# Kernel optimization log

Measured on AMD Instinct MI355X. Metric: run time of the kernel, lower is better.

## Reference

```python
import jax, jax.numpy as jnp
import numpy as np
import math

B, T, D, N = 4, 2048, 1024, 16
HD = D // N
SCALE = math.sqrt(D)  # source scales by sqrt(d_key) = sqrt(full model dim)
BIG = 1e9

def setup_inputs() -> dict:
    key = jax.random.key(0)
    ks = jax.random.split(key, 11)
    s = 1.0 / math.sqrt(D)
    return {
        "query": jax.random.normal(ks[0], (B, T, D), jnp.float32),
        "key": jax.random.normal(ks[1], (B, T, D), jnp.float32),
        "value": jax.random.normal(ks[2], (B, T, D), jnp.float32),
        "wq_w": jax.random.normal(ks[3], (D, D), jnp.float32) * s,
        "wq_b": jnp.zeros((D,), jnp.float32),
        "wk_w": jax.random.normal(ks[4], (D, D), jnp.float32) * s,
        "wk_b": jnp.zeros((D,), jnp.float32),
        "wv_w": jax.random.normal(ks[5], (D, D), jnp.float32) * s,
        "wv_b": jnp.zeros((D,), jnp.float32),
        "wo_w": jax.random.normal(ks[6], (D, D), jnp.float32) * s,
        "wo_b": jnp.zeros((D,), jnp.float32),
    }

def reference(query, key, value, wq_w, wq_b, wk_w, wk_b, wv_w, wv_b, wo_w, wo_b):
    # projections (torch Linear equiv; weights stored as (in,out))
    q = query @ wq_w + wq_b
    k = key @ wk_w + wk_b
    v = value @ wv_w + wv_b
    # split heads: (B,T,D) -> (B,N,T,HD)
    def split(x):
        return x.reshape(B, T, N, HD).transpose(0, 2, 1, 3)
    q, k, v = split(q), split(k), split(v)
    # dot products (source does elementwise mul+sum == einsum)
    scores = jnp.einsum('bnqd,bnkd->bnqk', q, k)
    # only_attend_front: subtract 1e9 on strict upper triangle
    tri = jnp.triu(jnp.ones((T, T), scores.dtype), 1) * BIG
    scores = scores - tri
    logits = scores / SCALE
    probs = jax.nn.softmax(logits, axis=-1)
    # zero rows where every position is masked (source trick)
    alive = ((scores <= -BIG / 2).sum(-1, keepdims=True) < T).astype(probs.dtype)
    probs = probs * alive
    out = jnp.einsum('bnqk,bnkd->bnqd', probs, v)  # (B,N,T,HD)
    out = out.transpose(0, 2, 1, 3).reshape(B, T, D)
    return out @ wo_w + wo_b
```

## Files before the change

kernel.cpp:

```cpp
#include <hip/hip_runtime.h>
#include <hip/hip_bf16.h>

#define BB 4
#define TT 2048
#define DD 1024
#define NHEAD 16
#define HDIM 64

typedef __bf16 v8bf __attribute__((ext_vector_type(8)));
typedef __bf16 v4bf __attribute__((ext_vector_type(4)));
typedef float  v4f  __attribute__((ext_vector_type(4)));

#define C2SCALE 0.04508422376f

__device__ __forceinline__ void gl2lds16(const void* g, void* l) {
  __builtin_amdgcn_global_load_lds(
      (__attribute__((address_space(1))) const void*)g,
      (__attribute__((address_space(3))) void*)l, 16, 0, 0);
}

__global__ __launch_bounds__(256) void prep(
    const float* __restrict__ qsrc, const float* __restrict__ ksrc,
    const float* __restrict__ vsrc,
    const float* __restrict__ w0, const float* __restrict__ w1,
    const float* __restrict__ w2, const float* __restrict__ w3,
    __bf16* __restrict__ qdst, __bf16* __restrict__ kdst,
    __bf16* __restrict__ vdst,
    __bf16* __restrict__ t0, __bf16* __restrict__ t1,
    __bf16* __restrict__ t2, __bf16* __restrict__ t3) {
  constexpr int STR = 72;
  __shared__ __bf16 sh[64 * STR];
  int bx = blockIdx.x, tid = threadIdx.x;
  if (bx < 12288) {
    const float* src = bx < 4096 ? qsrc : bx < 8192 ? ksrc : vsrc;
    __bf16* dst = bx < 4096 ? qdst : bx < 8192 ? kdst : vdst;
    int i = (bx & 4095) * 256 + tid;
    const float4* s = (const float4*)src + (size_t)i * 2;
    float4 f0 = s[0], f1 = s[1];
    v8bf v;
    v[0] = (__bf16)f0.x; v[1] = (__bf16)f0.y; v[2] = (__bf16)f0.z; v[3] = (__bf16)f0.w;
    v[4] = (__bf16)f1.x; v[5] = (__bf16)f1.y; v[6] = (__bf16)f1.z; v[7] = (__bf16)f1.w;
    *(v8bf*)(dst + (size_t)i * 8) = v;
  } else {
    int idx = bx - 12288;
    int z = idx >> 8;
    const float* W = z == 0 ? w0 : z == 1 ? w1 : z == 2 ? w2 : w3;
    __bf16* Wt = z == 0 ? t0 : z == 1 ? t1 : z == 2 ? t2 : t3;
    int n0 = (idx & 15) * 64, k0 = ((idx >> 4) & 15) * 64;
#pragma unroll
    for (int p = 0; p < 4; ++p) {
      int c = tid + p * 256;
      int r = c >> 4, off = (c & 15) * 4;
      float4 f = *(const float4*)(W + (size_t)(k0 + r) * DD + n0 + off);
      __bf16* d = &sh[r * STR + off];
      d[0] = (__bf16)f.x; d[1] = (__bf16)f.y; d[2] = (__bf16)f.z; d[3] = (__bf16)f.w;
    }
    __syncthreads();
#pragma unroll
    for (int p = 0; p < 2; ++p) {
      int c = tid + p * 256;
      int nr = c >> 3, koff = (c & 7) * 8;
      v8bf v;
#pragma unroll
      for (int j = 0; j < 8; ++j) v[j] = sh[(koff + j) * STR + nr];
      *(v8bf*)(Wt + (size_t)(n0 + nr) * DD + k0 + koff) = v;
    }
  }
}

__device__ __forceinline__ void gemm_core(const __bf16* __restrict__ A,
                                          const __bf16* __restrict__ Wt,
                                          int m0, int n0,
                                          __bf16* ash, __bf16* bsh,
                                          int wave, int lane, int quad, int l15,
                                          v4f acc[4][4]) {
  int wm = (wave & 1) * 64, wn = (wave >> 1) * 64;
  for (int k0 = 0; k0 < DD; k0 += 64) {
    __syncthreads();
#pragma unroll
    for (int i = 0; i < 4; ++i) {
      int c = wave * 256 + i * 64 + lane;
      int row = c >> 3, g = (c & 7) ^ (row & 7);
      gl2lds16(A + (size_t)(m0 + row) * DD + k0 + g * 8, ash + wave * 2048 + i * 512);
      gl2lds16(Wt + (size_t)(n0 + row) * DD + k0 + g * 8, bsh + wave * 2048 + i * 512);
    }
    __syncthreads();
#pragma unroll
    for (int ks = 0; ks < 2; ++ks) {
      int sw = (((ks * 4 + quad) ^ (l15 & 7))) * 8;
      v8bf a[4], b[4];
#pragma unroll
      for (int jm = 0; jm < 4; ++jm) a[jm] = *(v8bf*)&ash[(wm + jm * 16 + l15) * 64 + sw];
#pragma unroll
      for (int jn = 0; jn < 4; ++jn) b[jn] = *(v8bf*)&bsh[(wn + jn * 16 + l15) * 64 + sw];
#pragma unroll
      for (int jm = 0; jm < 4; ++jm)
#pragma unroll
        for (int jn = 0; jn < 4; ++jn)
          acc[jm][jn] = __builtin_amdgcn_mfma_f32_16x16x32_bf16(a[jm], b[jn], acc[jm][jn], 0, 0, 0);
    }
  }
}

__device__ __forceinline__ void swz_tiles(int& m0, int& n0) {
  int lin = blockIdx.x + 8 * blockIdx.y;
  int c = lin & 7, t = lin >> 3;
  n0 = (t & 7) * 128;
  m0 = (c + ((t >> 3) << 3)) * 128;
}

__global__ __launch_bounds__(256) void gemm_qkv(
    const __bf16* __restrict__ Qc, const __bf16* __restrict__ Kc,
    const __bf16* __restrict__ Vc,
    const __bf16* __restrict__ wqT, const __bf16* __restrict__ wkT,
    const __bf16* __restrict__ wvT,
    const float* __restrict__ qb, const float* __restrict__ kb,
    const float* __restrict__ vb,
    __bf16* __restrict__ Qp, __bf16* __restrict__ Kp, __bf16* __restrict__ VTb) {
  __shared__ __bf16 ash[128 * 64];
  __shared__ __bf16 bsh[128 * 64];
  int z = blockIdx.z;
  const __bf16* A  = z == 0 ? Qc : z == 1 ? Kc : Vc;
  const __bf16* Wt = z == 0 ? wqT : z == 1 ? wkT : wvT;
  const float* bias = z == 0 ? qb : z == 1 ? kb : vb;
  int tid = threadIdx.x, wave = tid >> 6, lane = tid & 63;
  int quad = lane >> 4, l15 = lane & 15;
  int m0, n0;
  swz_tiles(m0, n0);
  int wm = (wave & 1) * 64, wn = (wave >> 1) * 64;
  v4f acc[4][4];
#pragma unroll
  for (int jm = 0; jm < 4; ++jm)
#pragma unroll
    for (int jn = 0; jn < 4; ++jn) acc[jm][jn] = (v4f){0.f, 0.f, 0.f, 0.f};

  gemm_core(A, Wt, m0, n0, ash, bsh, wave, lane, quad, l15, acc);

  if (z == 2) {
    int b = m0 >> 11;
    int tbase = (m0 & 2047) + wm;
#pragma unroll
    for (int jn = 0; jn < 4; ++jn) {
      int col = n0 + wn + jn * 16 + l15;
      float bv = bias[col];
      __bf16* rowp = VTb + ((size_t)(b * 16 + (col >> 6)) * 64 + (col & 63)) * TT;
#pragma unroll
      for (int jm = 0; jm < 4; ++jm) {
        v4bf o;
#pragma unroll
        for (int r = 0; r < 4; ++r) o[r] = (__bf16)(acc[jm][jn][r] + bv);
        *(v4bf*)(rowp + tbase + jm * 16 + quad * 4) = o;
      }
    }
  } else {
    __bf16* C = z == 0 ? Qp : Kp;
    float scale = z == 0 ? C2SCALE : 1.0f;
#pragma unroll
    for (int jn = 0; jn < 4; ++jn) {
      int col = n0 + wn + jn * 16 + l15;
      float bv = bias[col];
#pragma unroll
      for (int jm = 0; jm < 4; ++jm) {
#pragma unroll
        for (int r = 0; r < 4; ++r) {
          int row = m0 + wm + jm * 16 + quad * 4 + r;
          C[(size_t)row * DD + col] = (__bf16)((acc[jm][jn][r] + bv) * scale);
        }
      }
    }
  }
}

__global__ __launch_bounds__(256) void gemm_out(const __bf16* __restrict__ A,
                                                const __bf16* __restrict__ Wt,
                                                const float* __restrict__ bias,
                                                float* __restrict__ C) {
  __shared__ __bf16 ash[128 * 64];
  __shared__ __bf16 bsh[128 * 64];
  int tid = threadIdx.x, wave = tid >> 6, lane = tid & 63;
  int quad = lane >> 4, l15 = lane & 15;
  int m0, n0;
  swz_tiles(m0, n0);
  int wm = (wave & 1) * 64, wn = (wave >> 1) * 64;
  v4f acc[4][4];
#pragma unroll
  for (int jm = 0; jm < 4; ++jm)
#pragma unroll
    for (int jn = 0; jn < 4; ++jn) acc[jm][jn] = (v4f){0.f, 0.f, 0.f, 0.f};

  gemm_core(A, Wt, m0, n0, ash, bsh, wave, lane, quad, l15, acc);

#pragma unroll
  for (int jn = 0; jn < 4; ++jn) {
    int col = n0 + wn + jn * 16 + l15;
    float bv = bias[col];
#pragma unroll
    for (int jm = 0; jm < 4; ++jm) {
#pragma unroll
      for (int r = 0; r < 4; ++r) {
        int row = m0 + wm + jm * 16 + quad * 4 + r;
        C[(size_t)row * DD + col] = acc[jm][jn][r] + bv;
      }
    }
  }
}

__global__ __launch_bounds__(256) void attn_bal(const __bf16* __restrict__ Q,
                                                const __bf16* __restrict__ K,
                                                const __bf16* __restrict__ VT,
                                                __bf16* __restrict__ O) {
  __shared__ __bf16 ksh[64 * 64];
  __shared__ __bf16 vsh[64 * 64];
  __shared__ __bf16 psh[128 * 64];
  int tid = threadIdx.x, wave = tid >> 6, lane = tid & 63;
  int quad = lane >> 4, l15 = lane & 15;
  int swz = l15 & 7;
  int lin = blockIdx.x + 8 * blockIdx.y;
  int c = lin & 7, t = lin >> 3;
  int xq = t & 7;
  int bh = c + ((t >> 3) << 3);
  int b = bh >> 4, h = bh & 15;
  const __bf16* Qb = Q + (size_t)(b * TT) * DD + h * HDIM;
  const __bf16* Kb = K + (size_t)(b * TT) * DD + h * HDIM;
  const __bf16* Vb = VT + (size_t)bh * HDIM * TT;
  __bf16* Ob = O + (size_t)(b * TT) * DD + h * HDIM;

  for (int phase = 0; phase < 2; ++phase) {
    int qi = phase ? 15 - xq : xq;
    int q0 = qi * 128;

#pragma unroll
    for (int i = 0; i < 4; ++i) {
      int cc = wave * 256 + i * 64 + lane;
      int row = cc >> 3, g = (cc & 7) ^ (row & 7);
      gl2lds16(Qb + (size_t)(q0 + row) * DD + g * 8, psh + wave * 2048 + i * 512);
    }
    __builtin_amdgcn_s_waitcnt(0);

    v8bf qf[2][2];
#pragma unroll
    for (int set = 0; set < 2; ++set)
#pragma unroll
      for (int ks = 0; ks < 2; ++ks)
        qf[set][ks] = *(v8bf*)&psh[(wave * 32 + set * 16 + l15) * 64 + ((ks * 4 + quad) ^ swz) * 8];

    int qg[2] = {q0 + wave * 32 + l15, q0 + wave * 32 + 16 + l15};
    float lr[2] = {0.f, 0.f};
    v4f oacc[2][4];
#pragma unroll
    for (int set = 0; set < 2; ++set)
#pragma unroll
      for (int jm = 0; jm < 4; ++jm) oacc[set][jm] = (v4f){0.f, 0.f, 0.f, 0.f};

    int ktiles = 2 * qi + 2;
    for (int kt = 0; kt < ktiles; ++kt) {
      int k0 = kt * 64;
      __syncthreads();
#pragma unroll
      for (int i = 0; i < 2; ++i) {
        int cc = wave * 128 + i * 64 + lane;
        int row = cc >> 3, g = (cc & 7) ^ (row & 7);
        gl2lds16(Kb + (size_t)(k0 + row) * DD + g * 8, ksh + wave * 1024 + i * 512);
        gl2lds16(Vb + (size_t)row * TT + k0 + g * 8, vsh + wave * 1024 + i * 512);
      }
      __syncthreads();

      v4f s[2][4];
#pragma unroll
      for (int set = 0; set < 2; ++set)
#pragma unroll
        for (int jf = 0; jf < 4; ++jf) s[set][jf] = (v4f){0.f, 0.f, 0.f, 0.f};
#pragma unroll
      for (int ks = 0; ks < 2; ++ks) {
        int sw = ((ks * 4 + quad) ^ swz) * 8;
#pragma unroll
        for (int jf = 0; jf < 4; ++jf) {
          v8bf kf = *(v8bf*)&ksh[(jf * 16 + l15) * 64 + sw];
          s[0][jf] = __builtin_amdgcn_mfma_f32_16x16x32_bf16(kf, qf[0][ks], s[0][jf], 0, 0, 0);
          s[1][jf] = __builtin_amdgcn_mfma_f32_16x16x32_bf16(kf, qf[1][ks], s[1][jf], 0, 0, 0);
        }
      }

      bool diag = (kt >= 2 * qi);
#pragma unroll
      for (int set = 0; set < 2; ++set) {
        int qrow = wave * 32 + set * 16 + l15;
        __bf16* prow = &psh[qrow * 64];
#pragma unroll
        for (int jf = 0; jf < 4; ++jf) {
          v4bf pk;
#pragma unroll
          for (int r = 0; r < 4; ++r) {
            float p = __builtin_amdgcn_exp2f(s[set][jf][r]);
            if (diag) {
              int kg = k0 + jf * 16 + quad * 4 + r;
              if (kg > qg[set]) p = 0.f;
            }
            lr[set] += p;
            pk[r] = (__bf16)p;
          }
          int chunk = jf * 2 + (quad >> 1);
          *(v4bf*)&prow[(chunk ^ swz) * 8 + (quad & 1) * 4] = pk;
        }
      }

#pragma unroll
      for (int ks = 0; ks < 2; ++ks) {
        int sw = ((ks * 4 + quad) ^ swz) * 8;
        v8bf pb0 = *(v8bf*)&psh[(wave * 32 + l15) * 64 + sw];
        v8bf pb1 = *(v8bf*)&psh[(wave * 32 + 16 + l15) * 64 + sw];
#pragma unroll
        for (int jm = 0; jm < 4; ++jm) {
          v8bf vf = *(v8bf*)&vsh[(jm * 16 + l15) * 64 + sw];
          oacc[0][jm] = __builtin_amdgcn_mfma_f32_16x16x32_bf16(vf, pb0, oacc[0][jm], 0, 0, 0);
          oacc[1][jm] = __builtin_amdgcn_mfma_f32_16x16x32_bf16(vf, pb1, oacc[1][jm], 0, 0, 0);
        }
      }
    }

#pragma unroll
    for (int set = 0; set < 2; ++set) {
      float l = lr[set];
      l += __shfl_xor(l, 16, 64);
      l += __shfl_xor(l, 32, 64);
      float inv = 1.0f / l;
      int q = q0 + wave * 32 + set * 16 + l15;
#pragma unroll
      for (int jm = 0; jm < 4; ++jm) {
        v4bf o;
#pragma unroll
        for (int r = 0; r < 4; ++r) o[r] = (__bf16)(oacc[set][jm][r] * inv);
        *(v4bf*)(Ob + (size_t)q * DD + jm * 16 + quad * 4) = o;
      }
    }
  }
}

extern "C" void kernel_launch(void* const* d_in, const int* in_sizes, int n_in,
                              void* d_out, int out_size, void* d_ws, size_t ws_size,
                              hipStream_t stream) {
  const float* query = (const float*)d_in[0];
  const float* key_  = (const float*)d_in[1];
  const float* value = (const float*)d_in[2];
  const float* wq_w = (const float*)d_in[3];
  const float* wq_b = (const float*)d_in[4];
  const float* wk_w = (const float*)d_in[5];
  const float* wk_b = (const float*)d_in[6];
  const float* wv_w = (const float*)d_in[7];
  const float* wv_b = (const float*)d_in[8];
  const float* wo_w = (const float*)d_in[9];
  const float* wo_b = (const float*)d_in[10];

  char* ws = (char*)d_ws;
  const size_t MB = (size_t)1 << 20;
  __bf16* wqT = (__bf16*)(ws + 0 * MB);
  __bf16* wkT = (__bf16*)(ws + 2 * MB);
  __bf16* wvT = (__bf16*)(ws + 4 * MB);
  __bf16* woT = (__bf16*)(ws + 6 * MB);
  __bf16* Qc  = (__bf16*)(ws + 8 * MB);
  __bf16* Kc  = (__bf16*)(ws + 24 * MB);
  __bf16* Vc  = (__bf16*)(ws + 40 * MB);
  __bf16* Qp  = (__bf16*)(ws + 56 * MB);
  __bf16* Kp  = (__bf16*)(ws + 72 * MB);
  __bf16* VTb = (__bf16*)(ws + 88 * MB);
  __bf16* Ab  = (__bf16*)(ws + 8 * MB);
  float* out = (float*)d_out;

  dim3 tb(256);
  prep<<<dim3(13312), tb, 0, stream>>>(query, key_, value, wq_w, wk_w, wv_w, wo_w,
                                       Qc, Kc, Vc, wqT, wkT, wvT, woT);
  gemm_qkv<<<dim3(8, 64, 3), tb, 0, stream>>>(Qc, Kc, Vc, wqT, wkT, wvT,
                                              wq_b, wk_b, wv_b, Qp, Kp, VTb);
  attn_bal<<<dim3(8, 64), tb, 0, stream>>>(Qp, Kp, VTb, Ab);
  gemm_out<<<dim3(8, 64), tb, 0, stream>>>(Ab, woT, wo_b, out);
}
```

Before: 322.1 us.

## Double-buffer K/V tiles in attention and compute row sums via MFMA

Adds a second LDS buffer for K and V so the next tile's global-to-LDS loads are issued before the current tile is computed, with a single wait and barrier at the end of each iteration. This is meant to hide global load latency behind the QK and PV matrix work. It also replaces the per-lane scalar accumulation of softmax denominators, and the shuffle reduction that followed, with an MFMA against a vector of ones on the bf16 probabilities. That removes VALU adds but sums the bf16-rounded values instead of fp32 ones, and doubles K/V LDS use, which may reduce occupancy.

```diff
diff --git a/kernel.cpp b/kernel.cpp
--- a/kernel.cpp
+++ b/kernel.cpp
@@ -209,8 +209,8 @@
                                                 const __bf16* __restrict__ K,
                                                 const __bf16* __restrict__ VT,
                                                 __bf16* __restrict__ O) {
-  __shared__ __bf16 ksh[64 * 64];
-  __shared__ __bf16 vsh[64 * 64];
+  __shared__ __bf16 ksh[2][64 * 64];
+  __shared__ __bf16 vsh[2][64 * 64];
   __shared__ __bf16 psh[128 * 64];
   int tid = threadIdx.x, wave = tid >> 6, lane = tid & 63;
   int quad = lane >> 4, l15 = lane & 15;
@@ -225,9 +225,14 @@
   const __bf16* Vb = VT + (size_t)bh * HDIM * TT;
   __bf16* Ob = O + (size_t)(b * TT) * DD + h * HDIM;
 
+  v8bf ones;
+#pragma unroll
+  for (int j = 0; j < 8; ++j) ones[j] = (__bf16)1.0f;
+
   for (int phase = 0; phase < 2; ++phase) {
     int qi = phase ? 15 - xq : xq;
     int q0 = qi * 128;
+    int ktiles = 2 * qi + 2;
 
 #pragma unroll
     for (int i = 0; i < 4; ++i) {
@@ -235,7 +240,15 @@
       int row = cc >> 3, g = (cc & 7) ^ (row & 7);
       gl2lds16(Qb + (size_t)(q0 + row) * DD + g * 8, psh + wave * 2048 + i * 512);
     }
+#pragma unroll
+    for (int i = 0; i < 2; ++i) {
+      int cc = wave * 128 + i * 64 + lane;
+      int row = cc >> 3, g = (cc & 7) ^ (row & 7);
+      gl2lds16(Kb + (size_t)row * DD + g * 8, &ksh[0][wave * 1024 + i * 512]);
+      gl2lds16(Vb + (size_t)row * TT + g * 8, &vsh[0][wave * 1024 + i * 512]);
+    }
     __builtin_amdgcn_s_waitcnt(0);
+    __syncthreads();
 
     v8bf qf[2][2];
 #pragma unroll
@@ -245,25 +258,29 @@
         qf[set][ks] = *(v8bf*)&psh[(wave * 32 + set * 16 + l15) * 64 + ((ks * 4 + quad) ^ swz) * 8];
 
     int qg[2] = {q0 + wave * 32 + l15, q0 + wave * 32 + 16 + l15};
-    float lr[2] = {0.f, 0.f};
-    v4f oacc[2][4];
-#pragma unroll
-    for (int set = 0; set < 2; ++set)
+    v4f oacc[2][4], lracc[2];
+#pragma unroll
+    for (int set = 0; set < 2; ++set) {
+      lracc[set] = (v4f){0.f, 0.f, 0.f, 0.f};
 #pragma unroll
       for (int jm = 0; jm < 4; ++jm) oacc[set][jm] = (v4f){0.f, 0.f, 0.f, 0.f};
-
-    int ktiles = 2 * qi + 2;
+    }
+
+    int pbuf = 0;
     for (int kt = 0; kt < ktiles; ++kt) {
+      if (kt + 1 < ktiles) {
+        int k0n = (kt + 1) * 64;
+#pragma unroll
+        for (int i = 0; i < 2; ++i) {
+          int cc = wave * 128 + i * 64 + lane;
+          int row = cc >> 3, g = (cc & 7) ^ (row & 7);
+          gl2lds16(Kb + (size_t)(k0n + row) * DD + g * 8, &ksh[pbuf ^ 1][wave * 1024 + i * 512]);
+          gl2lds16(Vb + (size_t)row * TT + k0n + g * 8, &vsh[pbuf ^ 1][wave * 1024 + i * 512]);
+        }
+      }
       int k0 = kt * 64;
-      __syncthreads();
-#pragma unroll
-      for (int i = 0; i < 2; ++i) {
-        int cc = wave * 128 + i * 64 + lane;
-        int row = cc >> 3, g = (cc & 7) ^ (row & 7);
-        gl2lds16(Kb + (size_t)(k0 + row) * DD + g * 8, ksh + wave * 1024 + i * 512);
-        gl2lds16(Vb + (size_t)row * TT + k0 + g * 8, vsh + wave * 1024 + i * 512);
-      }
-      __syncthreads();
+      const __bf16* kshp = &ksh[pbuf][0];
+      const __bf16* vshp = &vsh[pbuf][0];
 
       v4f s[2][4];
 #pragma unroll
@@ -275,7 +292,7 @@
         int sw = ((ks * 4 + quad) ^ swz) * 8;
 #pragma unroll
         for (int jf = 0; jf < 4; ++jf) {
-          v8bf kf = *(v8bf*)&ksh[(jf * 16 + l15) * 64 + sw];
+          v8bf kf = *(v8bf*)&kshp[(jf * 16 + l15) * 64 + sw];
           s[0][jf] = __builtin_amdgcn_mfma_f32_16x16x32_bf16(kf, qf[0][ks], s[0][jf], 0, 0, 0);
           s[1][jf] = __builtin_amdgcn_mfma_f32_16x16x32_bf16(kf, qf[1][ks], s[1][jf], 0, 0, 0);
         }
@@ -296,7 +313,6 @@
               int kg = k0 + jf * 16 + quad * 4 + r;
               if (kg > qg[set]) p = 0.f;
             }
-            lr[set] += p;
             pk[r] = (__bf16)p;
           }
           int chunk = jf * 2 + (quad >> 1);
@@ -309,21 +325,24 @@
         int sw = ((ks * 4 + quad) ^ swz) * 8;
         v8bf pb0 = *(v8bf*)&psh[(wave * 32 + l15) * 64 + sw];
         v8bf pb1 = *(v8bf*)&psh[(wave * 32 + 16 + l15) * 64 + sw];
+        lracc[0] = __builtin_amdgcn_mfma_f32_16x16x32_bf16(ones, pb0, lracc[0], 0, 0, 0);
+        lracc[1] = __builtin_amdgcn_mfma_f32_16x16x32_bf16(ones, pb1, lracc[1], 0, 0, 0);
 #pragma unroll
         for (int jm = 0; jm < 4; ++jm) {
-          v8bf vf = *(v8bf*)&vsh[(jm * 16 + l15) * 64 + sw];
+          v8bf vf = *(v8bf*)&vshp[(jm * 16 + l15) * 64 + sw];
           oacc[0][jm] = __builtin_amdgcn_mfma_f32_16x16x32_bf16(vf, pb0, oacc[0][jm], 0, 0, 0);
           oacc[1][jm] = __builtin_amdgcn_mfma_f32_16x16x32_bf16(vf, pb1, oacc[1][jm], 0, 0, 0);
         }
       }
+
+      __builtin_amdgcn_s_waitcnt(0);
+      __syncthreads();
+      pbuf ^= 1;
     }
 
 #pragma unroll
     for (int set = 0; set < 2; ++set) {
-      float l = lr[set];
-      l += __shfl_xor(l, 16, 64);
-      l += __shfl_xor(l, 32, 64);
-      float inv = 1.0f / l;
+      float inv = 1.0f / lracc[set][0];
       int q = q0 + wave * 32 + set * 16 + l15;
 #pragma unroll
       for (int jm = 0; jm < 4; ++jm) {
```

New measurement: 317.0 us. Within noise of the previous version (-1.6%).
